# Performance work log

Hardware: AMD Instinct MI355X
Metric: run time of the kernel (lower is better)

## Reference

```python
import jax, jax.numpy as jnp
import numpy as np

B, S, HID, NH, INTER = 1, 2048, 1024, 16, 4096
D = INTER // NH  # per-head intermediate dim = 256


def setup_inputs() -> dict:
    key = jax.random.key(0)
    ks = jax.random.split(key, 10)
    w = lambda k, shp: jax.random.normal(k, shp, jnp.float32) * 0.02
    return {
        "x": jax.random.normal(ks[0], (B, S, HID), jnp.float32),
        "adjacency": jax.random.uniform(ks[1], (B, NH, S, S), jnp.float32),
        "Wg": w(ks[2], (INTER, HID)),   # gate_proj.weight (out,in)
        "Wu": w(ks[3], (INTER, HID)),   # up_proj.weight
        "Wd": w(ks[4], (HID, INTER)),   # down_proj.weight
        "eps": jnp.zeros((NH,), jnp.float32),   # GIN epsilons (init 0)
        "alpha": jnp.ones((NH,), jnp.float32),  # sum-agg scales (init 1)
        "Wq": w(ks[5], (NH, D, D)),     # per-head attn_query_projs weights (out,in)
        "Wk": w(ks[6], (NH, D, D)),     # per-head attn_key_projs weights
        "W1": w(ks[7], (D, 4 * D)),     # aggregator_mlp[0].weight
        "W2": w(ks[8], (D, D)),         # aggregator_mlp[2].weight
    }


def reference(x, adjacency, Wg, Wu, Wd, eps, alpha, Wq, Wk, W1, W2):
    b, s, _ = x.shape
    nh, d, _ = Wq.shape
    # first half of SwiGLU MLP
    h = jax.nn.silu(x @ Wg.T) * (x @ Wu.T)            # (b, s, inter)
    h = h.reshape(b, s, nh, d).transpose(0, 2, 1, 3)  # (b, h, s, d)
    # GIN original term
    orig = (1.0 + eps)[None, :, None, None] * h
    # sum aggregation over adjacency
    sum_agg = alpha[None, :, None, None] * jnp.einsum('bhij,bhjd->bhid', adjacency, h)
    # max over identical expanded copies of h along the neighbor axis == h itself
    max_agg = h
    # adjacency-log-masked attention aggregation
    Q = jnp.einsum('bhsd,hed->bhse', h, Wq)
    K = jnp.einsum('bhsd,hed->bhse', h, Wk)
    scores = jnp.einsum('bhse,bhte->bhst', Q, K) / jnp.sqrt(jnp.float32(d))
    scores = scores + jnp.log(adjacency + 1e-9)
    attn = jax.nn.softmax(scores, axis=-1)
    attn_agg = jnp.einsum('bhst,bhtd->bhsd', attn, h)
    # 4-way concat + aggregator MLP (per head, shared weights)
    comb = jnp.concatenate([orig, sum_agg, max_agg, attn_agg], axis=-1)  # (b,h,s,4d)
    gin = jnp.einsum('bhsd,od->bhso', jax.nn.silu(jnp.einsum('bhsi,oi->bhso', comb, W1)), W2)
    # recombine heads and finish MLP
    gin = gin.transpose(0, 2, 1, 3).reshape(b, s, nh * d)
    return gin @ Wd.T
```

## Files before the change

### kernel.cpp

```cpp
#include <hip/hip_runtime.h>

typedef unsigned short u16;
typedef __attribute__((ext_vector_type(4))) float f32x4;
typedef __attribute__((ext_vector_type(8))) short s16x8;
typedef __attribute__((ext_vector_type(4))) short s16x4;

#define DEVI static __device__ __forceinline__

constexpr int S = 2048, HID = 1024, NH = 16, D = 256, INTER = 4096;

constexpr size_t N_XB   = (size_t)S*HID;
constexpr size_t N_W    = (size_t)INTER*HID;
constexpr size_t N_WQK  = (size_t)NH*D*D;
constexpr size_t N_W1C  = (size_t)NH*D*768;
constexpr size_t N_W2   = (size_t)D*D;
constexpr size_t N_COMB = (size_t)NH*S*768;
constexpr size_t N_HB   = (size_t)NH*S*D;

constexpr size_t O_XB   = 0;
constexpr size_t O_WG   = O_XB + N_XB;
constexpr size_t O_WU   = O_WG + N_W;
constexpr size_t O_WD   = O_WU + N_W;
constexpr size_t O_WQ   = O_WD + N_W;
constexpr size_t O_WK   = O_WQ + N_WQK;
constexpr size_t O_W1C  = O_WK + N_WQK;
constexpr size_t O_W2   = O_W1C + N_W1C;
constexpr size_t O_COMB = O_W2 + N_W2;
constexpr size_t O_HB   = O_COMB + N_COMB;
constexpr size_t O_QB   = O_HB + N_HB;
constexpr size_t O_KC   = O_QB + N_HB;

DEVI u16 f2bf(float f) {
  union { float f; unsigned u; } v; v.f = f;
  unsigned r = v.u + 0x7FFFu + ((v.u >> 16) & 1u);
  return (u16)(r >> 16);
}

DEVI float bf2f(u16 b) {
  union { unsigned u; float f; } v; v.u = ((unsigned)b) << 16;
  return v.f;
}

DEVI void gload16(const void* g, const void* l) {
  __builtin_amdgcn_global_load_lds(
      (const __attribute__((address_space(1))) unsigned int*)g,
      (__attribute__((address_space(3))) unsigned int*)l, 16, 0, 0);
}

DEVI f32x4 ntload(const float* p) {
  return __builtin_nontemporal_load((const f32x4*)p);
}

DEVI void stage_rm(const u16* src, int stride, u16* lds, int tid) {
  const int wid = tid >> 6;
#pragma unroll
  for (int i = 0; i < 2; ++i) {
    int c = i * 256 + tid;
    gload16(src + (size_t)(c & 127) * stride + (c >> 7) * 8,
            lds + (size_t)(i * 256 + wid * 64) * 8);
  }
}

DEVI void stage_rm64(const u16* src, int stride, u16* lds, int tid) {
  const int wid = tid >> 6;
  gload16(src + (size_t)(tid & 63) * stride + (tid >> 6) * 8,
          lds + (size_t)(wid * 64) * 8);
}

DEVI s16x8 ldfrag(const u16* lds, int kp, int row) {
  return *(const s16x8*)(lds + ((size_t)kp * 128 + row) * 8);
}

DEVI s16x8 ldfrag64(const u16* lds, int kp, int row) {
  return *(const s16x8*)(lds + ((size_t)kp * 64 + row) * 8);
}

__global__ void k_convert(const float* __restrict__ x,  const float* __restrict__ Wg,
                          const float* __restrict__ Wu, const float* __restrict__ Wd,
                          const float* __restrict__ Wq, const float* __restrict__ Wk,
                          const float* __restrict__ W1, const float* __restrict__ W2,
                          const float* __restrict__ eps, const float* __restrict__ alpha,
                          u16* __restrict__ ws) {
  const size_t totv = (N_XB + 3 * N_W + 2 * N_WQK) / 4;
  for (size_t vi = (size_t)blockIdx.x * blockDim.x + threadIdx.x; vi < totv;
       vi += (size_t)gridDim.x * blockDim.x) {
    size_t j = vi * 4;
    const float* src; size_t dst;
    if (j < N_XB)                { src = x  + j;                    dst = O_XB + j; }
    else if ((j -= N_XB) < N_W)  { src = Wg + j;                    dst = O_WG + j; }
    else if ((j -= N_W) < N_W)   { src = Wu + j;                    dst = O_WU + j; }
    else if ((j -= N_W) < N_W)   { src = Wd + j;                    dst = O_WD + j; }
    else if ((j -= N_W) < N_WQK) { src = Wq + j;                    dst = O_WQ + j; }
    else   { j -= N_WQK;           src = Wk + j;                    dst = O_WK + j; }
    f32x4 v = *(const f32x4*)src;
    s16x4 w;
    w[0] = (short)f2bf(v[0]); w[1] = (short)f2bf(v[1]);
    w[2] = (short)f2bf(v[2]); w[3] = (short)f2bf(v[3]);
    *(s16x4*)(ws + dst) = w;
  }
  const size_t tot2 = N_W2 + N_W1C;
  for (size_t i = (size_t)blockIdx.x * blockDim.x + threadIdx.x; i < tot2;
       i += (size_t)gridDim.x * blockDim.x) {
    size_t j = i;
    if (j < N_W2) { ws[O_W2 + j] = f2bf(W2[(j % D) * D + (j / D)]); continue; } j -= N_W2;
    size_t h = j / ((size_t)D * 768);
    size_t r = j % ((size_t)D * 768);
    size_t o = r / 768, c = r % 768;
    float v;
    if (c < 256)      v = (1.f + eps[h]) * W1[o * 1024 + c] + W1[o * 1024 + 512 + c];
    else if (c < 512) v = alpha[h] * W1[o * 1024 + c];
    else              v = W1[o * 1024 + 256 + c];
    ws[O_W1C + j] = f2bf(v);
  }
}

template <int MODE>
__global__ __launch_bounds__(256, 2) void k_dual(const u16* __restrict__ Ab,
                                                 const u16* __restrict__ B0b,
                                                 const u16* __restrict__ B1b,
                                                 u16* __restrict__ o0, u16* __restrict__ o1) {
  __shared__ u16 lA[4096], lB0[4096], lB1[4096];
  const int tid = threadIdx.x, lane = tid & 63, wid = tid >> 6;
  const int wm = wid >> 1, wn = wid & 1;
  int m0, nt, head;
  {
    const int bid = blockIdx.x, slot = bid & 7, j = bid >> 3;
    if (MODE == 0) {
      nt   = slot * 4 + (j & 3);
      m0   = (j >> 2) * 128;
      head = 0;
    } else {
      head = slot + 8 * (j >> 5);
      const int rem = j & 31;
      nt   = rem & 1;
      m0   = (rem >> 1) * 128;
    }
  }

  const int K  = (MODE == 0) ? HID : D;
  const int sA = (MODE == 0) ? HID : 768;
  const int sB = (MODE == 0) ? HID : D;
  const u16* A  = (MODE == 0) ? (Ab + (size_t)m0 * HID)
                              : (Ab + ((size_t)head * S + m0) * 768);
  const u16* B0 = (MODE == 0) ? (B0b + (size_t)nt * 128 * HID)
                              : (B0b + (size_t)head * D * D + (size_t)nt * 128 * D);
  const u16* B1 = (MODE == 0) ? (B1b + (size_t)nt * 128 * HID)
                              : (B1b + (size_t)head * D * D + (size_t)nt * 128 * D);

  f32x4 a0[4][4], a1[4][4];
#pragma unroll
  for (int i = 0; i < 4; ++i)
#pragma unroll
    for (int j2 = 0; j2 < 4; ++j2) { a0[i][j2] = f32x4{0.f,0.f,0.f,0.f}; a1[i][j2] = f32x4{0.f,0.f,0.f,0.f}; }

  for (int k0 = 0; k0 < K; k0 += 32) {
    __syncthreads();
    stage_rm(A  + k0, sA, lA,  tid);
    stage_rm(B0 + k0, sB, lB0, tid);
    stage_rm(B1 + k0, sB, lB1, tid);
    __syncthreads();
    const int kp = lane >> 4, r = lane & 15;
    s16x8 af[4], b0f[4], b1f[4];
#pragma unroll
    for (int f = 0; f < 4; ++f) {
      af[f]  = ldfrag(lA,  kp, wm * 64 + f * 16 + r);
      b0f[f] = ldfrag(lB0, kp, wn * 64 + f * 16 + r);
      b1f[f] = ldfrag(lB1, kp, wn * 64 + f * 16 + r);
    }
#pragma unroll
    for (int fi = 0; fi < 4; ++fi)
#pragma unroll
      for (int fj = 0; fj < 4; ++fj) {
        a0[fi][fj] = __builtin_amdgcn_mfma_f32_16x16x32_bf16(af[fi], b0f[fj], a0[fi][fj], 0, 0, 0);
        a1[fi][fj] = __builtin_amdgcn_mfma_f32_16x16x32_bf16(af[fi], b1f[fj], a1[fi][fj], 0, 0, 0);
      }
  }

#pragma unroll
  for (int fi = 0; fi < 4; ++fi)
#pragma unroll
    for (int fj = 0; fj < 4; ++fj)
#pragma unroll
      for (int reg = 0; reg < 4; ++reg) {
        int row = m0 + wm * 64 + fi * 16 + ((lane >> 4) * 4 + reg);
        int cl  = wn * 64 + fj * 16 + (lane & 15);
        if (MODE == 0) {
          int col = nt * 128 + cl;
          float g = a0[fi][fj][reg], uu = a1[fi][fj][reg];
          float h = g / (1.f + __expf(-g)) * uu;
          u16 hb = f2bf(h);
          int hh = col >> 8, d = col & 255;
          o0[((size_t)hh * S + row) * 768 + d] = hb;
          o1[(((size_t)hh * (S / 8) + (row >> 3)) * 256 + d) * 8 + (row & 7)] = hb;
        } else {
          int e = nt * 128 + cl;
          o0[((size_t)head * S + row) * D + e] = f2bf(a0[fi][fj][reg]);
          o1[(((size_t)head * 32 + (e >> 3)) * S + row) * 8 + (e & 7)] = f2bf(a1[fi][fj][reg]);
        }
      }
}

__global__ __launch_bounds__(256, 2) void k_attn(const float* __restrict__ adj,
                                                 const u16* __restrict__ Qb,
                                                 const u16* __restrict__ Kc,
                                                 const u16* __restrict__ hB,
                                                 u16* __restrict__ comb) {
  __shared__ u16 lK[2][1024 * 8];
  __shared__ u16 lH[2][1024 * 8];
  __shared__ u16 lAdj[2][64 * 36];
  __shared__ u16 lP[4][16 * 36];
  const int tid = threadIdx.x, lane = tid & 63, wid = tid >> 6;
  const int bid  = blockIdx.x;
  const int slot = bid & 7;
  const int idx  = bid >> 3;
  const int head = slot + 8 * (idx >> 5);
  const int bx   = idx & 31;
  const int q0 = bx * 64 + wid * 16;
  const int l15 = lane & 15, l4 = lane >> 4;

  s16x8 q[8];
  {
    const u16* qr = Qb + ((size_t)head * S + q0 + l15) * D + l4 * 8;
#pragma unroll
    for (int ks = 0; ks < 8; ++ks) q[ks] = *(const s16x8*)(qr + ks * 32);
  }
  f32x4 accO[16], accS[16];
#pragma unroll
  for (int i = 0; i < 16; ++i) { accO[i] = f32x4{0.f,0.f,0.f,0.f}; accS[i] = f32x4{0.f,0.f,0.f,0.f}; }
  float m_r[4] = {-1e30f, -1e30f, -1e30f, -1e30f};
  float l_r[4] = {0.f, 0.f, 0.f, 0.f};

  const float* adjB = adj + ((size_t)head * S + bx * 64) * S;
  const int arow = tid >> 3;
  const int acol = (tid & 7) * 4;

#pragma unroll
  for (int i = 0; i < 4; ++i) {
    int c = i * 256 + tid;
    gload16(Kc + ((size_t)(head * 32 + (c >> 5)) * S + (c & 31)) * 8,
            &lK[0][(size_t)(i * 256 + wid * 64) * 8]);
  }
#pragma unroll
  for (int i = 0; i < 4; ++i) {
    int c = i * 256 + tid;
    gload16(hB + ((size_t)(head * (S / 8) + (c >> 8)) * 256 + (c & 255)) * 8,
            &lH[0][(size_t)(i * 256 + wid * 64) * 8]);
  }
  f32x4 av0 = ntload(adjB + (size_t)arow * S + acol);
  f32x4 av1 = ntload(adjB + (size_t)(arow + 32) * S + acol);

  auto TILE = [&](int t0, int cur) {
    const int t1 = (t0 + 32 < S) ? t0 + 32 : t0;
#pragma unroll
    for (int i = 0; i < 4; ++i) {
      int c = i * 256 + tid;
      gload16(Kc + ((size_t)(head * 32 + (c >> 5)) * S + t1 + (c & 31)) * 8,
              &lK[cur ^ 1][(size_t)(i * 256 + wid * 64) * 8]);
    }
#pragma unroll
    for (int i = 0; i < 4; ++i) {
      int c = i * 256 + tid;
      gload16(hB + ((size_t)(head * (S / 8) + (t1 >> 3) + (c >> 8)) * 256 + (c & 255)) * 8,
              &lH[cur ^ 1][(size_t)(i * 256 + wid * 64) * 8]);
    }
    f32x4 nv0 = ntload(adjB + (size_t)arow * S + t1 + acol);
    f32x4 nv1 = ntload(adjB + (size_t)(arow + 32) * S + t1 + acol);
    {
      s16x4 w;
      w[0] = (short)f2bf(av0[0]); w[1] = (short)f2bf(av0[1]);
      w[2] = (short)f2bf(av0[2]); w[3] = (short)f2bf(av0[3]);
      *(s16x4*)(&lAdj[cur][(size_t)arow * 36 + acol]) = w;
      w[0] = (short)f2bf(av1[0]); w[1] = (short)f2bf(av1[1]);
      w[2] = (short)f2bf(av1[2]); w[3] = (short)f2bf(av1[3]);
      *(s16x4*)(&lAdj[cur][(size_t)(arow + 32) * 36 + acol]) = w;
    }
    asm volatile("s_waitcnt vmcnt(10) lgkmcnt(0)" ::: "memory");
    __builtin_amdgcn_s_barrier();
    __builtin_amdgcn_sched_barrier(0);

    const u16* lKc = &lK[cur][0];
    const u16* lHc = &lH[cur][0];
    const u16* lAc = &lAdj[cur][0];

    f32x4 scA[2], scB[2];
    scA[0] = f32x4{0.f,0.f,0.f,0.f}; scA[1] = f32x4{0.f,0.f,0.f,0.f};
    scB[0] = f32x4{0.f,0.f,0.f,0.f}; scB[1] = f32x4{0.f,0.f,0.f,0.f};
#pragma unroll
    for (int ks = 0; ks < 4; ++ks)
#pragma unroll
      for (int fj = 0; fj < 2; ++fj) {
        s16x8 b0 = *(const s16x8*)(lKc + ((size_t)(ks * 4 + l4) * 32 + fj * 16 + l15) * 8);
        s16x8 b1 = *(const s16x8*)(lKc + ((size_t)((ks + 4) * 4 + l4) * 32 + fj * 16 + l15) * 8);
        scA[fj] = __builtin_amdgcn_mfma_f32_16x16x32_bf16(q[ks], b0, scA[fj], 0, 0, 0);
        scB[fj] = __builtin_amdgcn_mfma_f32_16x16x32_bf16(q[ks + 4], b1, scB[fj], 0, 0, 0);
      }

    float av[2][4];
#pragma unroll
    for (int fj = 0; fj < 2; ++fj)
#pragma unroll
      for (int reg = 0; reg < 4; ++reg)
        av[fj][reg] = bf2f(lAc[(size_t)(wid * 16 + l4 * 4 + reg) * 36 + fj * 16 + l15]);

    float sf[2][4];
#pragma unroll
    for (int fj = 0; fj < 2; ++fj)
#pragma unroll
      for (int reg = 0; reg < 4; ++reg)
        sf[fj][reg] = (scA[fj][reg] + scB[fj][reg]) * 0.0625f;

    bool chg = false;
    float lmax[4];
#pragma unroll
    for (int reg = 0; reg < 4; ++reg) {
      lmax[reg] = fmaxf(sf[0][reg], sf[1][reg]);
      chg |= (lmax[reg] > m_r[reg] + 8.f);
    }
    if (__any((int)chg)) {
      float scl[4];
#pragma unroll
      for (int reg = 0; reg < 4; ++reg) {
        float m = lmax[reg];
#pragma unroll
        for (int off = 1; off < 16; off <<= 1) m = fmaxf(m, __shfl_xor(m, off));
        float mn = fmaxf(m_r[reg], m);
        scl[reg] = __expf(m_r[reg] - mn);
        m_r[reg] = mn;
        l_r[reg] *= scl[reg];
      }
#pragma unroll
      for (int nf = 0; nf < 16; ++nf) {
        f32x4 t = accO[nf];
        t[0] *= scl[0]; t[1] *= scl[1]; t[2] *= scl[2]; t[3] *= scl[3];
        accO[nf] = t;
      }
    }
    u16 pb[2][4];
#pragma unroll
    for (int fj = 0; fj < 2; ++fj)
#pragma unroll
      for (int reg = 0; reg < 4; ++reg) {
        float p = (av[fj][reg] + 1e-9f) * exp2f((sf[fj][reg] - m_r[reg]) * 1.44269504f);
        l_r[reg] += p;
        pb[fj][reg] = f2bf(p);
      }

    u16* pl = &lP[wid][0];
#pragma unroll
    for (int fj = 0; fj < 2; ++fj)
#pragma unroll
      for (int reg = 0; reg < 4; ++reg)
        pl[(size_t)(l4 * 4 + reg) * 36 + fj * 16 + l15] = pb[fj][reg];
    asm volatile("s_waitcnt lgkmcnt(0)" ::: "memory");
    __builtin_amdgcn_sched_barrier(0);

    s16x8 pa, aa;
    {
      s16x4 plo = *(const s16x4*)(pl + (size_t)l15 * 36 + l4 * 8);
      s16x4 phi = *(const s16x4*)(pl + (size_t)l15 * 36 + l4 * 8 + 4);
      pa[0] = plo[0]; pa[1] = plo[1]; pa[2] = plo[2]; pa[3] = plo[3];
      pa[4] = phi[0]; pa[5] = phi[1]; pa[6] = phi[2]; pa[7] = phi[3];
      s16x4 alo = *(const s16x4*)(lAc + (size_t)(wid * 16 + l15) * 36 + l4 * 8);
      s16x4 ahi = *(const s16x4*)(lAc + (size_t)(wid * 16 + l15) * 36 + l4 * 8 + 4);
      aa[0] = alo[0]; aa[1] = alo[1]; aa[2] = alo[2]; aa[3] = alo[3];
      aa[4] = ahi[0]; aa[5] = ahi[1]; aa[6] = ahi[2]; aa[7] = ahi[3];
    }
#pragma unroll
    for (int nf = 0; nf < 16; ++nf) {
      s16x8 hb = *(const s16x8*)(lHc + ((size_t)l4 * 256 + nf * 16 + l15) * 8);
      accO[nf] = __builtin_amdgcn_mfma_f32_16x16x32_bf16(pa, hb, accO[nf], 0, 0, 0);
      accS[nf] = __builtin_amdgcn_mfma_f32_16x16x32_bf16(aa, hb, accS[nf], 0, 0, 0);
    }

    av0 = nv0; av1 = nv1;

    __builtin_amdgcn_sched_barrier(0);
    __builtin_amdgcn_s_barrier();
  };

  for (int t0 = 0; t0 < S; t0 += 64) {
    TILE(t0, 0);
    TILE(t0 + 32, 1);
  }

  asm volatile("s_waitcnt vmcnt(0)" ::: "memory");

#pragma unroll
  for (int reg = 0; reg < 4; ++reg) {
#pragma unroll
    for (int off = 1; off < 16; off <<= 1) l_r[reg] += __shfl_xor(l_r[reg], off);
  }
  float inv[4];
#pragma unroll
  for (int reg = 0; reg < 4; ++reg) inv[reg] = 1.f / l_r[reg];
#pragma unroll
  for (int nf = 0; nf < 16; ++nf)
#pragma unroll
    for (int reg = 0; reg < 4; ++reg) {
      size_t rb = ((size_t)head * S + q0 + l4 * 4 + reg) * 768;
      comb[rb + 512 + nf * 16 + l15] = f2bf(accO[nf][reg] * inv[reg]);
      comb[rb + 256 + nf * 16 + l15] = f2bf(accS[nf][reg]);
    }
}

template <int MODE>
__global__ __launch_bounds__(256, 2) void k_gemm(const u16* __restrict__ Ab,
                                                 const u16* __restrict__ Bb,
                                                 u16* __restrict__ oU, float* __restrict__ oF) {
  constexpr int BN = (MODE == 2) ? 64 : 128;
  constexpr int FJ = BN / 32;
  __shared__ u16 lA[4096], lB[BN * 32];
  const int tid = threadIdx.x, lane = tid & 63, wid = tid >> 6;
  const int wm = wid >> 1, wn = wid & 1;
  int m0, nt, head;
  if constexpr (MODE == 0) {
    const int bid = blockIdx.x, slot = bid & 7, j = bid >> 3;
    head = slot + 8 * (j >> 5);
    const int rem = j & 31;
    nt   = rem & 1;
    m0   = (rem >> 1) * 128;
  } else if constexpr (MODE == 2) {
    const int bid = blockIdx.x, slot = bid & 7, j = bid >> 3;
    nt   = slot * 2 + (j & 1);
    m0   = (j >> 1) * 128;
    head = 0;
  } else {
    m0 = blockIdx.x * 128; nt = blockIdx.y; head = blockIdx.z;
  }

  constexpr int K  = (MODE == 0) ? 768 : (MODE == 2) ? INTER : D;
  constexpr int sA = (MODE == 3) ? INTER : K;
  constexpr int sB = K;
  const u16* A = (MODE == 0) ? Ab + ((size_t)head * S + m0) * 768
               : (MODE == 2) ? Ab + (size_t)m0 * INTER
                             : Ab + (size_t)m0 * INTER + head * D;
  const u16* B = (MODE == 0) ? Bb + ((size_t)head * D + nt * 128) * 768
                             : Bb + (size_t)nt * BN * sB;

  f32x4 acc[4][FJ];
#pragma unroll
  for (int i = 0; i < 4; ++i)
#pragma unroll
    for (int j = 0; j < FJ; ++j) acc[i][j] = f32x4{0.f,0.f,0.f,0.f};

  for (int k0 = 0; k0 < K; k0 += 32) {
    __syncthreads();
    stage_rm(A + k0, sA, lA, tid);
    if constexpr (BN == 128) stage_rm(B + k0, sB, lB, tid);
    else                     stage_rm64(B + k0, sB, lB, tid);
    __syncthreads();
    const int kp = lane >> 4, r = lane & 15;
    s16x8 af[4], bf[FJ];
#pragma unroll
    for (int f = 0; f < 4; ++f) af[f] = ldfrag(lA, kp, wm * 64 + f * 16 + r);
#pragma unroll
    for (int f = 0; f < FJ; ++f) {
      if constexpr (BN == 128) bf[f] = ldfrag(lB, kp, wn * 64 + f * 16 + r);
      else                     bf[f] = ldfrag64(lB, kp, wn * 32 + f * 16 + r);
    }
#pragma unroll
    for (int fi = 0; fi < 4; ++fi)
#pragma unroll
      for (int fj = 0; fj < FJ; ++fj)
        acc[fi][fj] = __builtin_amdgcn_mfma_f32_16x16x32_bf16(af[fi], bf[fj], acc[fi][fj], 0, 0, 0);
  }

#pragma unroll
  for (int fi = 0; fi < 4; ++fi)
#pragma unroll
    for (int fj = 0; fj < FJ; ++fj)
#pragma unroll
      for (int reg = 0; reg < 4; ++reg) {
        int row = m0 + wm * 64 + fi * 16 + ((lane >> 4) * 4 + reg);
        int cn = nt * BN + wn * (BN / 2) + fj * 16 + (lane & 15);
        float v = acc[fi][fj][reg];
        if (MODE == 0) {
          v = v / (1.f + __expf(-v));
          oU[(size_t)row * INTER + head * D + cn] = f2bf(v);
        } else if (MODE == 3) {
          oU[(size_t)row * INTER + head * D + cn] = f2bf(v);
        } else {
          oF[(size_t)row * HID + cn] = v;
        }
      }
}

extern "C" void kernel_launch(void* const* d_in, const int* in_sizes, int n_in,
                              void* d_out, int out_size, void* d_ws, size_t ws_size,
                              hipStream_t stream) {
  const float* x     = (const float*)d_in[0];
  const float* adj   = (const float*)d_in[1];
  const float* Wg    = (const float*)d_in[2];
  const float* Wu    = (const float*)d_in[3];
  const float* Wd    = (const float*)d_in[4];
  const float* eps   = (const float*)d_in[5];
  const float* alpha = (const float*)d_in[6];
  const float* Wq    = (const float*)d_in[7];
  const float* Wk    = (const float*)d_in[8];
  const float* W1    = (const float*)d_in[9];
  const float* W2    = (const float*)d_in[10];
  u16* ws = (u16*)d_ws;

  k_convert<<<dim3(4096), dim3(256), 0, stream>>>(x, Wg, Wu, Wd, Wq, Wk, W1, W2, eps, alpha, ws);
  k_dual<0><<<dim3(512), dim3(256), 0, stream>>>(ws + O_XB, ws + O_WG, ws + O_WU,
                                                 ws + O_COMB, ws + O_HB);
  k_dual<1><<<dim3(512), dim3(256), 0, stream>>>(ws + O_COMB, ws + O_WQ, ws + O_WK,
                                                 ws + O_QB, ws + O_KC);
  k_attn<<<dim3(512), dim3(256), 0, stream>>>(adj, ws + O_QB, ws + O_KC, ws + O_HB, ws + O_COMB);
  k_gemm<3><<<dim3(8, 2, 16), dim3(256), 0, stream>>>(ws + O_WD, ws + O_W2, ws + O_KC, nullptr);
  k_gemm<0><<<dim3(512), dim3(256), 0, stream>>>(ws + O_COMB, ws + O_W1C, ws + O_QB, nullptr);
  k_gemm<2><<<dim3(256), dim3(256), 0, stream>>>(ws + O_QB, ws + O_KC, nullptr, (float*)d_out);
}
```

Before: 381.5 us.

## Double-buffer LDS tiles in dual and generic GEMM kernels with prefetch

```diff
diff --git a/kernel.cpp b/kernel.cpp
--- a/kernel.cpp
+++ b/kernel.cpp
@@ -119,7 +119,7 @@
                                                  const u16* __restrict__ B0b,
                                                  const u16* __restrict__ B1b,
                                                  u16* __restrict__ o0, u16* __restrict__ o1) {
-  __shared__ u16 lA[4096], lB0[4096], lB1[4096];
+  __shared__ u16 lA[2][4096], lB0[2][4096], lB1[2][4096];
   const int tid = threadIdx.x, lane = tid & 63, wid = tid >> 6;
   const int wm = wid >> 1, wn = wid & 1;
   int m0, nt, head;
@@ -153,19 +153,24 @@
 #pragma unroll
     for (int j2 = 0; j2 < 4; ++j2) { a0[i][j2] = f32x4{0.f,0.f,0.f,0.f}; a1[i][j2] = f32x4{0.f,0.f,0.f,0.f}; }
 
-  for (int k0 = 0; k0 < K; k0 += 32) {
-    __syncthreads();
-    stage_rm(A  + k0, sA, lA,  tid);
-    stage_rm(B0 + k0, sB, lB0, tid);
-    stage_rm(B1 + k0, sB, lB1, tid);
-    __syncthreads();
+  auto STAGE = [&](int k0, int cur) {
+    stage_rm(A  + k0, sA, &lA[cur][0],  tid);
+    stage_rm(B0 + k0, sB, &lB0[cur][0], tid);
+    stage_rm(B1 + k0, sB, &lB1[cur][0], tid);
+  };
+  auto STEP = [&](int k0, int cur) {
+    const int k1 = (k0 + 32 < K) ? k0 + 32 : k0;
+    STAGE(k1, cur ^ 1);
+    asm volatile("s_waitcnt vmcnt(6)" ::: "memory");
+    __builtin_amdgcn_s_barrier();
+    __builtin_amdgcn_sched_barrier(0);
     const int kp = lane >> 4, r = lane & 15;
     s16x8 af[4], b0f[4], b1f[4];
 #pragma unroll
     for (int f = 0; f < 4; ++f) {
-      af[f]  = ldfrag(lA,  kp, wm * 64 + f * 16 + r);
-      b0f[f] = ldfrag(lB0, kp, wn * 64 + f * 16 + r);
-      b1f[f] = ldfrag(lB1, kp, wn * 64 + f * 16 + r);
+      af[f]  = ldfrag(&lA[cur][0],  kp, wm * 64 + f * 16 + r);
+      b0f[f] = ldfrag(&lB0[cur][0], kp, wn * 64 + f * 16 + r);
+      b1f[f] = ldfrag(&lB1[cur][0], kp, wn * 64 + f * 16 + r);
     }
 #pragma unroll
     for (int fi = 0; fi < 4; ++fi)
@@ -174,7 +179,13 @@
         a0[fi][fj] = __builtin_amdgcn_mfma_f32_16x16x32_bf16(af[fi], b0f[fj], a0[fi][fj], 0, 0, 0);
         a1[fi][fj] = __builtin_amdgcn_mfma_f32_16x16x32_bf16(af[fi], b1f[fj], a1[fi][fj], 0, 0, 0);
       }
-  }
+    __builtin_amdgcn_sched_barrier(0);
+    __builtin_amdgcn_s_barrier();
+  };
+
+  STAGE(0, 0);
+  for (int k0 = 0; k0 < K; k0 += 64) { STEP(k0, 0); STEP(k0 + 32, 1); }
+  asm volatile("s_waitcnt vmcnt(0)" ::: "memory");
 
 #pragma unroll
   for (int fi = 0; fi < 4; ++fi)
@@ -409,7 +420,8 @@
                                                  u16* __restrict__ oU, float* __restrict__ oF) {
   constexpr int BN = (MODE == 2) ? 64 : 128;
   constexpr int FJ = BN / 32;
-  __shared__ u16 lA[4096], lB[BN * 32];
+  constexpr int NLD = 2 + ((BN == 128) ? 2 : 1);
+  __shared__ u16 lA[2][4096], lB[2][BN * 32];
   const int tid = threadIdx.x, lane = tid & 63, wid = tid >> 6;
   const int wm = wid >> 1, wn = wid & 1;
   int m0, nt, head;
@@ -443,27 +455,39 @@
 #pragma unroll
     for (int j = 0; j < FJ; ++j) acc[i][j] = f32x4{0.f,0.f,0.f,0.f};
 
-  for (int k0 = 0; k0 < K; k0 += 32) {
-    __syncthreads();
-    stage_rm(A + k0, sA, lA, tid);
-    if constexpr (BN == 128) stage_rm(B + k0, sB, lB, tid);
-    else                     stage_rm64(B + k0, sB, lB, tid);
-    __syncthreads();
+  auto STAGE = [&](int k0, int cur) {
+    stage_rm(A + k0, sA, &lA[cur][0], tid);
+    if constexpr (BN == 128) stage_rm(B + k0, sB, &lB[cur][0], tid);
+    else                     stage_rm64(B + k0, sB, &lB[cur][0], tid);
+  };
+  auto STEP = [&](int k0, int cur) {
+    const int k1 = (k0 + 32 < K) ? k0 + 32 : k0;
+    STAGE(k1, cur ^ 1);
+    if constexpr (NLD == 4) asm volatile("s_waitcnt vmcnt(4)" ::: "memory");
+    else                    asm volatile("s_waitcnt vmcnt(3)" ::: "memory");
+    __builtin_amdgcn_s_barrier();
+    __builtin_amdgcn_sched_barrier(0);
     const int kp = lane >> 4, r = lane & 15;
     s16x8 af[4], bf[FJ];
 #pragma unroll
-    for (int f = 0; f < 4; ++f) af[f] = ldfrag(lA, kp, wm * 64 + f * 16 + r);
+    for (int f = 0; f < 4; ++f) af[f] = ldfrag(&lA[cur][0], kp, wm * 64 + f * 16 + r);
 #pragma unroll
     for (int f = 0; f < FJ; ++f) {
-      if constexpr (BN == 128) bf[f] = ldfrag(lB, kp, wn * 64 + f * 16 + r);
-      else                     bf[f] = ldfrag64(lB, kp, wn * 32 + f * 16 + r);
+      if constexpr (BN == 128) bf[f] = ldfrag(&lB[cur][0], kp, wn * 64 + f * 16 + r);
+      else                     bf[f] = ldfrag64(&lB[cur][0], kp, wn * 32 + f * 16 + r);
     }
 #pragma unroll
     for (int fi = 0; fi < 4; ++fi)
 #pragma unroll
       for (int fj = 0; fj < FJ; ++fj)
         acc[fi][fj] = __builtin_amdgcn_mfma_f32_16x16x32_bf16(af[fi], bf[fj], acc[fi][fj], 0, 0, 0);
-  }
+    __builtin_amdgcn_sched_barrier(0);
+    __builtin_amdgcn_s_barrier();
+  };
+
+  STAGE(0, 0);
+  for (int k0 = 0; k0 < K; k0 += 64) { STEP(k0, 0); STEP(k0 + 32, 1); }
+  asm volatile("s_waitcnt vmcnt(0)" ::: "memory");
 
 #pragma unroll
   for (int fi = 0; fi < 4; ++fi)
```

New measurement: 385.6 us. Within noise of the previous version (+1.1%).
